# Kernel optimization log

Measured on AMD Instinct MI355X. Metric: run time of the kernel, lower is better.

## Reference

```python
import jax, jax.numpy as jnp
import numpy as np

T, D, H, E, K = 8192, 512, 1024, 16, 2  # tokens, d_model, d_hidden, num_expert, top_k


def setup_inputs() -> dict:
    key = jax.random.key(0)
    ks = jax.random.split(key, 4)
    return {
        "x": jax.random.normal(ks[0], (T, D), jnp.float32),
        "Wg": jax.random.normal(ks[1], (D, E), jnp.float32) * (D ** -0.5),
        "bg": jnp.zeros((E,), jnp.float32),
        "W1": jax.random.normal(ks[2], (E, D, H), jnp.float32) * (D ** -0.5),
        "b1": jnp.zeros((E, H), jnp.float32),
        "W2": jax.random.normal(ks[3], (E, H, D), jnp.float32) * (H ** -0.5),
        "b2": jnp.zeros((E, D), jnp.float32),
    }


def _moe(x, Wg, bg, W1, b1, W2, b2):
    # NaiveGate: linear -> top-k -> softmax over the k selected logits
    logits = x @ Wg + bg                              # [T, E]
    top_val, top_idx = jax.lax.top_k(logits, K)       # [T, K]
    score = jax.nn.softmax(top_val, axis=-1)          # [T, K]
    # Dispatch + per-expert MLP + combine. Mathematically identical to the
    # scatter/grouped-GEMM/gather: for each expert, the per-token combine
    # weight is the gate score if the token routed there, else 0.
    out = jnp.zeros_like(x)
    for e in range(E):  # fixed small loop over structurally distinct experts
        h = jax.nn.gelu(x @ W1[e] + b1[e], approximate=False)  # [T, H]
        y = h @ W2[e] + b2[e]                                   # [T, D]
        w_e = jnp.sum(jnp.where(top_idx == e, score, 0.0), axis=-1)  # [T]
        out = out + w_e[:, None] * y
    return out


def reference(x, Wg, bg, W1, b1, W2, b2):
    return _moe(x, Wg, bg, W1, b1, W2, b2)
```

## Files before the change

### kernel.cpp

```cpp
#include <hip/hip_runtime.h>
#include <hip/hip_bf16.h>
#include <math.h>

#define TT 8192
#define DD 512
#define HH 1024
#define EE 16
#define NSLOT 18432
#define MAXTILES 144
#define BM 128
#define RETRYCAP 1024

typedef __attribute__((ext_vector_type(8))) short bf16x8;
typedef __attribute__((ext_vector_type(8))) unsigned short u16x8;
typedef __attribute__((ext_vector_type(4))) float f32x4;

__device__ __forceinline__ unsigned short f2bf(float f) {
  union { float f; unsigned u; } v; v.f = f;
  unsigned r = v.u + 0x7fffu + ((v.u >> 16) & 1u);
  return (unsigned short)(r >> 16);
}

__device__ __forceinline__ float bf2f(unsigned short u) {
  union { unsigned u; float f; } v; v.u = ((unsigned)u) << 16;
  return v.f;
}

__device__ __forceinline__ void gload16(const void* g, void* l) {
  __builtin_amdgcn_global_load_lds(
      (const __attribute__((address_space(1))) unsigned int*)g,
      (__attribute__((address_space(3))) unsigned int*)l, 16, 0, 0);
}

__device__ __forceinline__ float gelu_f(float v) {
  float s = fabsf(v) * 0.70710678118654752f;
  float t = 1.0f / (1.0f + 0.3275911f * s);
  float poly = t * (0.254829592f +
              t * (-0.284496736f +
              t * (1.421413741f +
              t * (-1.453152027f +
              t * 1.061405429f))));
  float erfa = 1.0f - poly * __expf(-s * s);
  float erfv = (v >= 0.f) ? erfa : -erfa;
  return 0.5f * v * (1.0f + erfv);
}

__global__ __launch_bounds__(256) void transpose_cv_kernel(
    const float* __restrict__ in, unsigned short* __restrict__ out, int R, int C) {
  int mat = blockIdx.z;
  int c0 = blockIdx.x * 64;
  int r0 = blockIdx.y * 64;
  const float* src = in + (size_t)mat * R * C;
  unsigned short* dst = out + (size_t)mat * R * C;
  __shared__ unsigned short t[64][68];
  int tid = threadIdx.x;
#pragma unroll
  for (int p = 0; p < 4; p++) {
    int r = tid >> 2;
    int c4 = (tid & 3) + p * 4;
    float4 v = *(const float4*)(src + (size_t)(r0 + r) * C + c0 + c4 * 4);
    t[c4 * 4 + 0][r] = f2bf(v.x);
    t[c4 * 4 + 1][r] = f2bf(v.y);
    t[c4 * 4 + 2][r] = f2bf(v.z);
    t[c4 * 4 + 3][r] = f2bf(v.w);
  }
  __syncthreads();
#pragma unroll
  for (int p = 0; p < 4; p++) {
    int oc = (tid >> 4) + p * 16;
    int ch = tid & 15;
    ushort4 v = *(ushort4*)(&t[oc][ch * 4]);
    *(ushort4*)(dst + (size_t)(c0 + oc) * R + r0 + ch * 4) = v;
  }
}

__global__ __launch_bounds__(256) void gate_mfma_kernel(
    const float* __restrict__ x, const float* __restrict__ Wg,
    const float* __restrict__ bg, unsigned short* __restrict__ xb,
    int* __restrict__ gate_e, float* __restrict__ gate_w,
    int* __restrict__ counts, int* __restrict__ nretry,
    int* __restrict__ retry) {
  __shared__ __align__(16) unsigned short As[128][40];
  __shared__ int cnt_s[EE];
  int tid = threadIdx.x;
  int lane = tid & 63;
  int wave = tid >> 6;
  int tok0 = blockIdx.x * 128;
  if (tid < EE) cnt_s[tid] = 0;
  int e = lane & 15;
  int kb = (lane >> 4) * 8;
  bf16x8 bfrag[16];
#pragma unroll
  for (int ks = 0; ks < 16; ks++) {
    int kbase = ks * 32 + kb;
#pragma unroll
    for (int j = 0; j < 8; j++)
      bfrag[ks][j] = (short)f2bf(Wg[(kbase + j) * EE + e]);
  }
  float bge = bg[e];
  f32x4 acc[2];
  {
    f32x4 z = {0.f, 0.f, 0.f, 0.f};
    acc[0] = z; acc[1] = z;
  }
  int srow = tid >> 1;
  int sc0 = (tid & 1) * 16;
  const float* xrow = x + (size_t)(tok0 + srow) * DD + sc0;
  unsigned short* xbrow = xb + (size_t)(tok0 + srow) * DD + sc0;
  for (int ks = 0; ks < 16; ks++) {
    int k0 = ks * 32;
    __syncthreads();
    float4 v0 = *(const float4*)(xrow + k0);
    float4 v1 = *(const float4*)(xrow + k0 + 4);
    float4 v2 = *(const float4*)(xrow + k0 + 8);
    float4 v3 = *(const float4*)(xrow + k0 + 12);
    u16x8 w0, w1;
    w0[0] = f2bf(v0.x); w0[1] = f2bf(v0.y); w0[2] = f2bf(v0.z); w0[3] = f2bf(v0.w);
    w0[4] = f2bf(v1.x); w0[5] = f2bf(v1.y); w0[6] = f2bf(v1.z); w0[7] = f2bf(v1.w);
    w1[0] = f2bf(v2.x); w1[1] = f2bf(v2.y); w1[2] = f2bf(v2.z); w1[3] = f2bf(v2.w);
    w1[4] = f2bf(v3.x); w1[5] = f2bf(v3.y); w1[6] = f2bf(v3.z); w1[7] = f2bf(v3.w);
    *(u16x8*)(xbrow + k0) = w0;
    *(u16x8*)(xbrow + k0 + 8) = w1;
    *(u16x8*)(&As[srow][sc0]) = w0;
    *(u16x8*)(&As[srow][sc0 + 8]) = w1;
    __syncthreads();
    bf16x8 a0 = *(const bf16x8*)(&As[wave * 32 + (lane & 15)][kb]);
    bf16x8 a1 = *(const bf16x8*)(&As[wave * 32 + 16 + (lane & 15)][kb]);
    acc[0] = __builtin_amdgcn_mfma_f32_16x16x32_bf16(a0, bfrag[ks], acc[0], 0, 0, 0);
    acc[1] = __builtin_amdgcn_mfma_f32_16x16x32_bf16(a1, bfrag[ks], acc[1], 0, 0, 0);
  }
#pragma unroll
  for (int m = 0; m < 2; m++) {
#pragma unroll
    for (int r = 0; r < 4; r++) {
      float lf = acc[m][r] + bge;
      float v1 = -1e30f, v2 = -1e30f, v3 = -1e30f;
      int i1 = 0, i2 = 0;
#pragma unroll
      for (int q = 0; q < EE; q++) {
        float v = __shfl(lf, (lane & 48) | q);
        if (v > v1) { v3 = v2; v2 = v1; i2 = i1; v1 = v; i1 = q; }
        else if (v > v2) { v3 = v2; v2 = v; i2 = q; }
        else if (v > v3) { v3 = v; }
      }
      if ((lane & 15) == 0) {
        int t2 = tok0 + wave * 32 + m * 16 + ((lane >> 4) << 2) + r;
        float p = expf(v2 - v1);
        float s = 1.0f / (1.0f + p);
        gate_e[t2 * 2] = i1;
        gate_e[t2 * 2 + 1] = i2;
        gate_w[t2 * 2] = s;
        gate_w[t2 * 2 + 1] = p * s;
        atomicAdd(&cnt_s[i1], 1);
        atomicAdd(&cnt_s[i2], 1);
        if (v2 - v3 < 0.02f) {
          int pos = atomicAdd(nretry, 1);
          if (pos < RETRYCAP) retry[pos] = t2;
        }
      }
    }
  }
  __syncthreads();
  if (tid < EE) atomicAdd(&counts[tid], cnt_s[tid]);
}

__global__ __launch_bounds__(256) void gatefix_kernel(
    const float* __restrict__ x, const float* __restrict__ Wg,
    const float* __restrict__ bg, const int* __restrict__ nretry,
    const int* __restrict__ retry, int* __restrict__ gate_e,
    float* __restrict__ gate_w, int* __restrict__ counts) {
  __shared__ float lg[16][17];
  __shared__ int toks[16];
  int tid = threadIdx.x;
  int sl = tid >> 4, e = tid & 15;
  int s = blockIdx.x * 16 + sl;
  int n = *nretry; if (n > RETRYCAP) n = RETRYCAP;
  int active = (s < n);
  int tok = 0;
  if (active) tok = retry[s];
  if (active) {
    const float* xr = x + (size_t)tok * DD;
    double a0 = 0.0, a1 = 0.0, a2 = 0.0, a3 = 0.0;
    for (int i = 0; i < DD / 4; i++) {
      a0 += (double)xr[i * 4 + 0] * (double)Wg[(i * 4 + 0) * EE + e];
      a1 += (double)xr[i * 4 + 1] * (double)Wg[(i * 4 + 1) * EE + e];
      a2 += (double)xr[i * 4 + 2] * (double)Wg[(i * 4 + 2) * EE + e];
      a3 += (double)xr[i * 4 + 3] * (double)Wg[(i * 4 + 3) * EE + e];
    }
    double acc = (a0 + a1) + (a2 + a3);
    lg[sl][e] = (float)(acc + (double)bg[e]);
    toks[sl] = tok;
  }
  __syncthreads();
  if (active && e == 0) {
    float v1 = -1e30f, v2 = -1e30f;
    int i1 = 0, i2 = 0;
#pragma unroll
    for (int q = 0; q < EE; q++) {
      float v = lg[sl][q];
      if (v > v1) { v2 = v1; i2 = i1; v1 = v; i1 = q; }
      else if (v > v2) { v2 = v; i2 = q; }
    }
    int t2 = toks[sl];
    int o1 = gate_e[t2 * 2], o2 = gate_e[t2 * 2 + 1];
    float p = expf(v2 - v1);
    float sc = 1.0f / (1.0f + p);
    gate_e[t2 * 2] = i1;
    gate_e[t2 * 2 + 1] = i2;
    gate_w[t2 * 2] = sc;
    gate_w[t2 * 2 + 1] = p * sc;
    if (o1 != i1 || o2 != i2) {
      atomicSub(&counts[o1], 1);
      atomicSub(&counts[o2], 1);
      atomicAdd(&counts[i1], 1);
      atomicAdd(&counts[i2], 1);
    }
  }
}

__global__ void scan_kernel(const int* __restrict__ counts, int* __restrict__ offs,
                            int* __restrict__ tile_expert, int* __restrict__ ntiles,
                            int* __restrict__ fill) {
  if (threadIdx.x == 0) {
    int off = 0, nt = 0;
    for (int e = 0; e < EE; e++) {
      offs[e] = off;
      fill[e] = 0;
      int tiles = (counts[e] + BM - 1) / BM;
      for (int t = 0; t < tiles; t++) tile_expert[nt++] = e;
      off += tiles * BM;
    }
    offs[EE] = off;
    ntiles[0] = nt;
  }
}

__global__ __launch_bounds__(256) void scatter_kernel(
    const int* __restrict__ gate_e, const float* __restrict__ gate_w,
    const int* __restrict__ offs, int* __restrict__ fill,
    int* __restrict__ slot_token, float* __restrict__ slot_w,
    int* __restrict__ slot_of) {
  __shared__ int lcnt[EE];
  __shared__ int lbase[EE];
  int tid = threadIdx.x;
  int t = blockIdx.x * 256 + tid;
  if (tid < EE) lcnt[tid] = 0;
  __syncthreads();
  int e0 = gate_e[t * 2], e1 = gate_e[t * 2 + 1];
  int p0 = atomicAdd(&lcnt[e0], 1);
  int p1 = atomicAdd(&lcnt[e1], 1);
  __syncthreads();
  if (tid < EE) lbase[tid] = atomicAdd(&fill[tid], lcnt[tid]);
  __syncthreads();
  int s0 = offs[e0] + lbase[e0] + p0;
  int s1 = offs[e1] + lbase[e1] + p1;
  slot_token[s0] = t;
  slot_w[s0] = gate_w[t * 2];
  slot_of[t * 2] = s0;
  slot_token[s1] = t;
  slot_w[s1] = gate_w[t * 2 + 1];
  slot_of[t * 2 + 1] = s1;
}

__global__ __launch_bounds__(256) void gemm1_kernel(
    const unsigned short* __restrict__ xb, const unsigned short* __restrict__ w1t,
    const float* __restrict__ b1, const int* __restrict__ slot_token,
    const int* __restrict__ tile_expert, const int* __restrict__ ntiles,
    unsigned short* __restrict__ hb) {
  int mt = blockIdx.y;
  if (mt >= ntiles[0]) return;
  int e = tile_expert[mt];
  int row0 = mt * BM;
  int n0 = blockIdx.x * 128;
  __shared__ unsigned short As[2][128][32];
  __shared__ unsigned short Bs[2][128][32];
  int tid = threadIdx.x;
  int lane = tid & 63;
  int wave = tid >> 6;
  int wm = wave >> 1, wn = wave & 1;
  int ra = tid >> 2, c = tid & 3;
  int tok_a = slot_token[row0 + ra]; if (tok_a < 0) tok_a = 0;
  int tok_b = slot_token[row0 + ra + 64]; if (tok_b < 0) tok_b = 0;
  const unsigned short* wbase = w1t + ((size_t)e * HH * DD);
  const unsigned short* gA0 = xb + (size_t)tok_a * DD + c * 8;
  const unsigned short* gA1 = xb + (size_t)tok_b * DD + c * 8;
  const unsigned short* gB0 = wbase + (size_t)(n0 + ra) * DD + c * 8;
  const unsigned short* gB1 = wbase + (size_t)(n0 + ra + 64) * DD + c * 8;
  f32x4 acc[4][4];
#pragma unroll
  for (int m = 0; m < 4; m++)
#pragma unroll
    for (int n = 0; n < 4; n++) {
      f32x4 z = {0.f, 0.f, 0.f, 0.f};
      acc[m][n] = z;
    }
  gload16(gA0, &As[0][ra][c * 8]);
  gload16(gA1, &As[0][ra + 64][c * 8]);
  gload16(gB0, &Bs[0][ra][c * 8]);
  gload16(gB1, &Bs[0][ra + 64][c * 8]);
  int cur = 0;
  for (int kk = 0; kk < DD / 32; kk++) {
    if (kk + 1 < DD / 32) {
      int k1 = (kk + 1) * 32;
      int nx = cur ^ 1;
      gload16(gA0 + k1, &As[nx][ra][c * 8]);
      gload16(gA1 + k1, &As[nx][ra + 64][c * 8]);
      gload16(gB0 + k1, &Bs[nx][ra][c * 8]);
      gload16(gB1 + k1, &Bs[nx][ra + 64][c * 8]);
      asm volatile("s_waitcnt vmcnt(4)" ::: "memory");
    } else {
      asm volatile("s_waitcnt vmcnt(0)" ::: "memory");
    }
    __builtin_amdgcn_s_barrier();
    bf16x8 a[4], b[4];
#pragma unroll
    for (int m = 0; m < 4; m++)
      a[m] = *(const bf16x8*)(&As[cur][wm * 64 + m * 16 + (lane & 15)][(lane >> 4) * 8]);
#pragma unroll
    for (int n = 0; n < 4; n++)
      b[n] = *(const bf16x8*)(&Bs[cur][wn * 64 + n * 16 + (lane & 15)][(lane >> 4) * 8]);
#pragma unroll
    for (int m = 0; m < 4; m++)
#pragma unroll
      for (int n = 0; n < 4; n++)
        acc[m][n] = __builtin_amdgcn_mfma_f32_16x16x32_bf16(a[m], b[n], acc[m][n], 0, 0, 0);
    asm volatile("" ::: "memory");
    __builtin_amdgcn_s_barrier();
    cur ^= 1;
  }
  const float* b1e = b1 + (size_t)e * HH;
#pragma unroll
  for (int m = 0; m < 4; m++) {
#pragma unroll
    for (int r = 0; r < 4; r++) {
      int slot = row0 + wm * 64 + m * 16 + ((lane >> 4) << 2) + r;
      unsigned short* hrow = hb + (size_t)slot * HH;
#pragma unroll
      for (int n = 0; n < 4; n++) {
        int hc = n0 + wn * 64 + n * 16 + (lane & 15);
        float v = acc[m][n][r] + b1e[hc];
        hrow[hc] = f2bf(gelu_f(v));
      }
    }
  }
}

template <int USE_Y>
__global__ __launch_bounds__(256) void gemm2_kernel(
    const unsigned short* __restrict__ hb, const unsigned short* __restrict__ w2t,
    const float* __restrict__ b2, const int* __restrict__ slot_token,
    const float* __restrict__ slot_w, const int* __restrict__ tile_expert,
    const int* __restrict__ ntiles, unsigned short* __restrict__ yw,
    float* __restrict__ out) {
  int mt = blockIdx.y;
  if (mt >= ntiles[0]) return;
  int e = tile_expert[mt];
  int row0 = mt * BM;
  int n0 = blockIdx.x * 128;
  __shared__ unsigned short As[2][128][32];
  __shared__ unsigned short Bs[2][128][32];
  int tid = threadIdx.x;
  int lane = tid & 63;
  int wave = tid >> 6;
  int wm = wave >> 1, wn = wave & 1;
  int ra = tid >> 2, c = tid & 3;
  const unsigned short* wbase = w2t + ((size_t)e * DD * HH);
  const unsigned short* gA0 = hb + (size_t)(row0 + ra) * HH + c * 8;
  const unsigned short* gA1 = hb + (size_t)(row0 + ra + 64) * HH + c * 8;
  const unsigned short* gB0 = wbase + (size_t)(n0 + ra) * HH + c * 8;
  const unsigned short* gB1 = wbase + (size_t)(n0 + ra + 64) * HH + c * 8;
  f32x4 acc[4][4];
#pragma unroll
  for (int m = 0; m < 4; m++)
#pragma unroll
    for (int n = 0; n < 4; n++) {
      f32x4 z = {0.f, 0.f, 0.f, 0.f};
      acc[m][n] = z;
    }
  gload16(gA0, &As[0][ra][c * 8]);
  gload16(gA1, &As[0][ra + 64][c * 8]);
  gload16(gB0, &Bs[0][ra][c * 8]);
  gload16(gB1, &Bs[0][ra + 64][c * 8]);
  int cur = 0;
  for (int kk = 0; kk < HH / 32; kk++) {
    if (kk + 1 < HH / 32) {
      int k1 = (kk + 1) * 32;
      int nx = cur ^ 1;
      gload16(gA0 + k1, &As[nx][ra][c * 8]);
      gload16(gA1 + k1, &As[nx][ra + 64][c * 8]);
      gload16(gB0 + k1, &Bs[nx][ra][c * 8]);
      gload16(gB1 + k1, &Bs[nx][ra + 64][c * 8]);
      asm volatile("s_waitcnt vmcnt(4)" ::: "memory");
    } else {
      asm volatile("s_waitcnt vmcnt(0)" ::: "memory");
    }
    __builtin_amdgcn_s_barrier();
    bf16x8 a[4], b[4];
#pragma unroll
    for (int m = 0; m < 4; m++)
      a[m] = *(const bf16x8*)(&As[cur][wm * 64 + m * 16 + (lane & 15)][(lane >> 4) * 8]);
#pragma unroll
    for (int n = 0; n < 4; n++)
      b[n] = *(const bf16x8*)(&Bs[cur][wn * 64 + n * 16 + (lane & 15)][(lane >> 4) * 8]);
#pragma unroll
    for (int m = 0; m < 4; m++)
#pragma unroll
      for (int n = 0; n < 4; n++)
        acc[m][n] = __builtin_amdgcn_mfma_f32_16x16x32_bf16(a[m], b[n], acc[m][n], 0, 0, 0);
    asm volatile("" ::: "memory");
    __builtin_amdgcn_s_barrier();
    cur ^= 1;
  }
  const float* b2e = b2 + (size_t)e * DD;
#pragma unroll
  for (int m = 0; m < 4; m++) {
#pragma unroll
    for (int r = 0; r < 4; r++) {
      int slot = row0 + wm * 64 + m * 16 + ((lane >> 4) << 2) + r;
      if (USE_Y) {
        float w = slot_w[slot];
        unsigned short* yrow = yw + (size_t)slot * DD;
#pragma unroll
        for (int n = 0; n < 4; n++) {
          int dc = n0 + wn * 64 + n * 16 + (lane & 15);
          yrow[dc] = f2bf(w * (acc[m][n][r] + b2e[dc]));
        }
      } else {
        int tok = slot_token[slot];
        if (tok >= 0) {
          float w = slot_w[slot];
          float* orow = out + (size_t)tok * DD;
#pragma unroll
          for (int n = 0; n < 4; n++) {
            int dc = n0 + wn * 64 + n * 16 + (lane & 15);
            float v = acc[m][n][r] + b2e[dc];
            atomicAdd(&orow[dc], w * v);
          }
        }
      }
    }
  }
}

__global__ __launch_bounds__(256) void combine_kernel(
    const unsigned short* __restrict__ yw, const int* __restrict__ slot_of,
    float* __restrict__ out) {
  int gid = blockIdx.x * 256 + threadIdx.x;
  int t = gid >> 6;
  int d0 = (gid & 63) * 8;
  int s1 = slot_of[t * 2], s2 = slot_of[t * 2 + 1];
  const ushort4* p1 = (const ushort4*)(yw + (size_t)s1 * DD + d0);
  const ushort4* p2 = (const ushort4*)(yw + (size_t)s2 * DD + d0);
  ushort4 a0 = p1[0], a1 = p1[1];
  ushort4 b0 = p2[0], b1 = p2[1];
  float4 o0, o1;
  o0.x = bf2f(a0.x) + bf2f(b0.x);
  o0.y = bf2f(a0.y) + bf2f(b0.y);
  o0.z = bf2f(a0.z) + bf2f(b0.z);
  o0.w = bf2f(a0.w) + bf2f(b0.w);
  o1.x = bf2f(a1.x) + bf2f(b1.x);
  o1.y = bf2f(a1.y) + bf2f(b1.y);
  o1.z = bf2f(a1.z) + bf2f(b1.z);
  o1.w = bf2f(a1.w) + bf2f(b1.w);
  float* orow = out + (size_t)t * DD + d0;
  ((float4*)orow)[0] = o0;
  ((float4*)orow)[1] = o1;
}

extern "C" void kernel_launch(void* const* d_in, const int* in_sizes, int n_in,
                              void* d_out, int out_size, void* d_ws, size_t ws_size,
                              hipStream_t stream) {
  const float* x  = (const float*)d_in[0];
  const float* Wg = (const float*)d_in[1];
  const float* bg = (const float*)d_in[2];
  const float* W1 = (const float*)d_in[3];
  const float* b1 = (const float*)d_in[4];
  const float* W2 = (const float*)d_in[5];
  const float* b2 = (const float*)d_in[6];
  float* out = (float*)d_out;

  uint8_t* w = (uint8_t*)d_ws;
  size_t o = 0;
  unsigned short* xb  = (unsigned short*)(w + o); o += (size_t)TT * DD * 2;
  unsigned short* w1t = (unsigned short*)(w + o); o += (size_t)EE * DD * HH * 2;
  unsigned short* w2t = (unsigned short*)(w + o); o += (size_t)EE * DD * HH * 2;
  unsigned short* hb  = (unsigned short*)(w + o); o += (size_t)NSLOT * HH * 2;
  int*   slot_token = (int*)(w + o);   o += (size_t)NSLOT * 4;
  float* slot_w     = (float*)(w + o); o += (size_t)NSLOT * 4;
  int*   slot_of    = (int*)(w + o);   o += (size_t)TT * 2 * 4;
  int*   gate_e     = (int*)(w + o);   o += (size_t)TT * 2 * 4;
  float* gate_w     = (float*)(w + o); o += (size_t)TT * 2 * 4;
  int*   counts     = (int*)(w + o);   o += 64;
  int*   nretry     = (int*)(w + o);   o += 64;
  int*   tile_expert= (int*)(w + o);   o += 640;
  int*   ntiles     = (int*)(w + o);   o += 64;
  int*   offs       = (int*)(w + o);   o += 128;
  int*   fill       = (int*)(w + o);   o += 64;
  int*   retry      = (int*)(w + o);   o += RETRYCAP * 4;
  unsigned short* yw = (unsigned short*)(w + o);
  size_t need_y = o + (size_t)NSLOT * DD * 2;
  int use_y = (ws_size >= need_y);

  hipMemsetAsync(counts, 0, 128, stream);
  hipMemsetAsync(slot_token, 0xFF, (size_t)NSLOT * 4, stream);
  if (!use_y) hipMemsetAsync(d_out, 0, (size_t)TT * DD * 4, stream);

  {
    dim3 g(HH / 64, DD / 64, EE);
    transpose_cv_kernel<<<g, 256, 0, stream>>>(W1, w1t, DD, HH);
  }
  {
    dim3 g(DD / 64, HH / 64, EE);
    transpose_cv_kernel<<<g, 256, 0, stream>>>(W2, w2t, HH, DD);
  }
  gate_mfma_kernel<<<TT / 128, 256, 0, stream>>>(x, Wg, bg, xb, gate_e, gate_w,
                                                 counts, nretry, retry);
  gatefix_kernel<<<RETRYCAP / 16, 256, 0, stream>>>(x, Wg, bg, nretry, retry,
                                                    gate_e, gate_w, counts);
  scan_kernel<<<1, 64, 0, stream>>>(counts, offs, tile_expert, ntiles, fill);
  scatter_kernel<<<TT / 256, 256, 0, stream>>>(gate_e, gate_w, offs, fill,
                                               slot_token, slot_w, slot_of);
  {
    dim3 g(HH / 128, MAXTILES);
    gemm1_kernel<<<g, 256, 0, stream>>>(xb, w1t, b1, slot_token, tile_expert, ntiles, hb);
  }
  {
    dim3 g(DD / 128, MAXTILES);
    if (use_y)
      gemm2_kernel<1><<<g, 256, 0, stream>>>(hb, w2t, b2, slot_token, slot_w,
                                             tile_expert, ntiles, yw, out);
    else
      gemm2_kernel<0><<<g, 256, 0, stream>>>(hb, w2t, b2, slot_token, slot_w,
                                             tile_expert, ntiles, yw, out);
  }
  if (use_y) {
    combine_kernel<<<TT * (DD / 8) / 256, 256, 0, stream>>>(yw, slot_of, out);
  }
}
```

Before: 181.7 us.

## Triple-buffer GEMM k-loop, fuse transposes, and drop scan kernel via inline tile decode

Both grouped GEMMs move from double to triple buffering of LDS tiles, issuing loads two k-steps ahead with adjusted waitcnt so more memory latency is hidden. The two weight transpose launches are merged into one grid, and the single-thread scan kernel is removed: scatter computes expert offsets in shared memory, and the GEMMs decode their tile's expert and row offset from counts directly. This cuts kernel launches and one serial kernel. In exchange it raises LDS use per block, which may lower occupancy, and adds a small 16-iteration decode loop per block. The counts memset grows to also clear fill.

```diff
diff --git a/kernel.cpp b/kernel.cpp
--- a/kernel.cpp
+++ b/kernel.cpp
@@ -45,15 +45,38 @@
   return 0.5f * v * (1.0f + erfv);
 }
 
+__device__ __forceinline__ int tile_decode(const int* __restrict__ counts,
+                                           int mt, int* e_out, int* row0_out) {
+  int off = 0, rem = mt;
+#pragma unroll
+  for (int q = 0; q < EE; q++) {
+    int tl = (counts[q] + BM - 1) / BM;
+    if (rem < tl) { *e_out = q; *row0_out = off + rem * BM; return 1; }
+    rem -= tl;
+    off += tl * BM;
+  }
+  return 0;
+}
+
 __global__ __launch_bounds__(256) void transpose_cv_kernel(
-    const float* __restrict__ in, unsigned short* __restrict__ out, int R, int C) {
-  int mat = blockIdx.z;
-  int c0 = blockIdx.x * 64;
-  int r0 = blockIdx.y * 64;
-  const float* src = in + (size_t)mat * R * C;
-  unsigned short* dst = out + (size_t)mat * R * C;
+    const float* __restrict__ W1, const float* __restrict__ W2,
+    unsigned short* __restrict__ w1t, unsigned short* __restrict__ w2t) {
   __shared__ unsigned short t[64][68];
+  int bid = blockIdx.x;
   int tid = threadIdx.x;
+  const float* src;
+  unsigned short* dst;
+  int R, C, c0, r0;
+  if (bid < 2048) {
+    int cx = bid & 15, ry = (bid >> 4) & 7, mat = bid >> 7;
+    src = W1 + (size_t)mat * DD * HH; dst = w1t + (size_t)mat * DD * HH;
+    R = DD; C = HH; c0 = cx * 64; r0 = ry * 64;
+  } else {
+    int b = bid - 2048;
+    int cx = b & 7, ry = (b >> 3) & 15, mat = b >> 7;
+    src = W2 + (size_t)mat * DD * HH; dst = w2t + (size_t)mat * DD * HH;
+    R = HH; C = DD; c0 = cx * 64; r0 = ry * 64;
+  }
 #pragma unroll
   for (int p = 0; p < 4; p++) {
     int r = tid >> 2;
@@ -218,33 +241,24 @@
   }
 }
 
-__global__ void scan_kernel(const int* __restrict__ counts, int* __restrict__ offs,
-                            int* __restrict__ tile_expert, int* __restrict__ ntiles,
-                            int* __restrict__ fill) {
-  if (threadIdx.x == 0) {
-    int off = 0, nt = 0;
-    for (int e = 0; e < EE; e++) {
-      offs[e] = off;
-      fill[e] = 0;
-      int tiles = (counts[e] + BM - 1) / BM;
-      for (int t = 0; t < tiles; t++) tile_expert[nt++] = e;
-      off += tiles * BM;
-    }
-    offs[EE] = off;
-    ntiles[0] = nt;
-  }
-}
-
 __global__ __launch_bounds__(256) void scatter_kernel(
     const int* __restrict__ gate_e, const float* __restrict__ gate_w,
-    const int* __restrict__ offs, int* __restrict__ fill,
+    const int* __restrict__ counts, int* __restrict__ fill,
     int* __restrict__ slot_token, float* __restrict__ slot_w,
     int* __restrict__ slot_of) {
   __shared__ int lcnt[EE];
   __shared__ int lbase[EE];
+  __shared__ int offs_s[EE];
   int tid = threadIdx.x;
   int t = blockIdx.x * 256 + tid;
   if (tid < EE) lcnt[tid] = 0;
+  if (tid == 0) {
+    int off = 0;
+    for (int q = 0; q < EE; q++) {
+      offs_s[q] = off;
+      off += ((counts[q] + BM - 1) / BM) * BM;
+    }
+  }
   __syncthreads();
   int e0 = gate_e[t * 2], e1 = gate_e[t * 2 + 1];
   int p0 = atomicAdd(&lcnt[e0], 1);
@@ -252,8 +266,8 @@
   __syncthreads();
   if (tid < EE) lbase[tid] = atomicAdd(&fill[tid], lcnt[tid]);
   __syncthreads();
-  int s0 = offs[e0] + lbase[e0] + p0;
-  int s1 = offs[e1] + lbase[e1] + p1;
+  int s0 = offs_s[e0] + lbase[e0] + p0;
+  int s1 = offs_s[e1] + lbase[e1] + p1;
   slot_token[s0] = t;
   slot_w[s0] = gate_w[t * 2];
   slot_of[t * 2] = s0;
@@ -265,15 +279,12 @@
 __global__ __launch_bounds__(256) void gemm1_kernel(
     const unsigned short* __restrict__ xb, const unsigned short* __restrict__ w1t,
     const float* __restrict__ b1, const int* __restrict__ slot_token,
-    const int* __restrict__ tile_expert, const int* __restrict__ ntiles,
-    unsigned short* __restrict__ hb) {
-  int mt = blockIdx.y;
-  if (mt >= ntiles[0]) return;
-  int e = tile_expert[mt];
-  int row0 = mt * BM;
+    const int* __restrict__ counts, unsigned short* __restrict__ hb) {
+  int e, row0;
+  if (!tile_decode(counts, blockIdx.y, &e, &row0)) return;
   int n0 = blockIdx.x * 128;
-  __shared__ unsigned short As[2][128][32];
-  __shared__ unsigned short Bs[2][128][32];
+  __shared__ unsigned short As[3][128][32];
+  __shared__ unsigned short Bs[3][128][32];
   int tid = threadIdx.x;
   int lane = tid & 63;
   int wave = tid >> 6;
@@ -294,19 +305,26 @@
       f32x4 z = {0.f, 0.f, 0.f, 0.f};
       acc[m][n] = z;
     }
-  gload16(gA0, &As[0][ra][c * 8]);
-  gload16(gA1, &As[0][ra + 64][c * 8]);
-  gload16(gB0, &Bs[0][ra][c * 8]);
-  gload16(gB1, &Bs[0][ra + 64][c * 8]);
-  int cur = 0;
-  for (int kk = 0; kk < DD / 32; kk++) {
-    if (kk + 1 < DD / 32) {
-      int k1 = (kk + 1) * 32;
-      int nx = cur ^ 1;
-      gload16(gA0 + k1, &As[nx][ra][c * 8]);
-      gload16(gA1 + k1, &As[nx][ra + 64][c * 8]);
-      gload16(gB0 + k1, &Bs[nx][ra][c * 8]);
-      gload16(gB1 + k1, &Bs[nx][ra + 64][c * 8]);
+  const int NK = DD / 32;
+#pragma unroll
+  for (int p = 0; p < 2; p++) {
+    int kj = p * 32;
+    gload16(gA0 + kj, &As[p][ra][c * 8]);
+    gload16(gA1 + kj, &As[p][ra + 64][c * 8]);
+    gload16(gB0 + kj, &Bs[p][ra][c * 8]);
+    gload16(gB1 + kj, &Bs[p][ra + 64][c * 8]);
+  }
+  for (int kk = 0; kk < NK; kk++) {
+    int cur = kk % 3;
+    if (kk + 2 < NK) {
+      int k2 = (kk + 2) * 32;
+      int nx = (kk + 2) % 3;
+      gload16(gA0 + k2, &As[nx][ra][c * 8]);
+      gload16(gA1 + k2, &As[nx][ra + 64][c * 8]);
+      gload16(gB0 + k2, &Bs[nx][ra][c * 8]);
+      gload16(gB1 + k2, &Bs[nx][ra + 64][c * 8]);
+      asm volatile("s_waitcnt vmcnt(8)" ::: "memory");
+    } else if (kk + 1 < NK) {
       asm volatile("s_waitcnt vmcnt(4)" ::: "memory");
     } else {
       asm volatile("s_waitcnt vmcnt(0)" ::: "memory");
@@ -326,7 +344,6 @@
         acc[m][n] = __builtin_amdgcn_mfma_f32_16x16x32_bf16(a[m], b[n], acc[m][n], 0, 0, 0);
     asm volatile("" ::: "memory");
     __builtin_amdgcn_s_barrier();
-    cur ^= 1;
   }
   const float* b1e = b1 + (size_t)e * HH;
 #pragma unroll
@@ -349,16 +366,13 @@
 __global__ __launch_bounds__(256) void gemm2_kernel(
     const unsigned short* __restrict__ hb, const unsigned short* __restrict__ w2t,
     const float* __restrict__ b2, const int* __restrict__ slot_token,
-    const float* __restrict__ slot_w, const int* __restrict__ tile_expert,
-    const int* __restrict__ ntiles, unsigned short* __restrict__ yw,
-    float* __restrict__ out) {
-  int mt = blockIdx.y;
-  if (mt >= ntiles[0]) return;
-  int e = tile_expert[mt];
-  int row0 = mt * BM;
+    const float* __restrict__ slot_w, const int* __restrict__ counts,
+    unsigned short* __restrict__ yw, float* __restrict__ out) {
+  int e, row0;
+  if (!tile_decode(counts, blockIdx.y, &e, &row0)) return;
   int n0 = blockIdx.x * 128;
-  __shared__ unsigned short As[2][128][32];
-  __shared__ unsigned short Bs[2][128][32];
+  __shared__ unsigned short As[3][128][32];
+  __shared__ unsigned short Bs[3][128][32];
   int tid = threadIdx.x;
   int lane = tid & 63;
   int wave = tid >> 6;
@@ -377,19 +391,26 @@
       f32x4 z = {0.f, 0.f, 0.f, 0.f};
       acc[m][n] = z;
     }
-  gload16(gA0, &As[0][ra][c * 8]);
-  gload16(gA1, &As[0][ra + 64][c * 8]);
-  gload16(gB0, &Bs[0][ra][c * 8]);
-  gload16(gB1, &Bs[0][ra + 64][c * 8]);
-  int cur = 0;
-  for (int kk = 0; kk < HH / 32; kk++) {
-    if (kk + 1 < HH / 32) {
-      int k1 = (kk + 1) * 32;
-      int nx = cur ^ 1;
-      gload16(gA0 + k1, &As[nx][ra][c * 8]);
-      gload16(gA1 + k1, &As[nx][ra + 64][c * 8]);
-      gload16(gB0 + k1, &Bs[nx][ra][c * 8]);
-      gload16(gB1 + k1, &Bs[nx][ra + 64][c * 8]);
+  const int NK = HH / 32;
+#pragma unroll
+  for (int p = 0; p < 2; p++) {
+    int kj = p * 32;
+    gload16(gA0 + kj, &As[p][ra][c * 8]);
+    gload16(gA1 + kj, &As[p][ra + 64][c * 8]);
+    gload16(gB0 + kj, &Bs[p][ra][c * 8]);
+    gload16(gB1 + kj, &Bs[p][ra + 64][c * 8]);
+  }
+  for (int kk = 0; kk < NK; kk++) {
+    int cur = kk % 3;
+    if (kk + 2 < NK) {
+      int k2 = (kk + 2) * 32;
+      int nx = (kk + 2) % 3;
+      gload16(gA0 + k2, &As[nx][ra][c * 8]);
+      gload16(gA1 + k2, &As[nx][ra + 64][c * 8]);
+      gload16(gB0 + k2, &Bs[nx][ra][c * 8]);
+      gload16(gB1 + k2, &Bs[nx][ra + 64][c * 8]);
+      asm volatile("s_waitcnt vmcnt(8)" ::: "memory");
+    } else if (kk + 1 < NK) {
       asm volatile("s_waitcnt vmcnt(4)" ::: "memory");
     } else {
       asm volatile("s_waitcnt vmcnt(0)" ::: "memory");
@@ -409,7 +430,6 @@
         acc[m][n] = __builtin_amdgcn_mfma_f32_16x16x32_bf16(a[m], b[n], acc[m][n], 0, 0, 0);
     asm volatile("" ::: "memory");
     __builtin_amdgcn_s_barrier();
-    cur ^= 1;
   }
   const float* b2e = b2 + (size_t)e * DD;
 #pragma unroll
@@ -492,46 +512,35 @@
   float* gate_w     = (float*)(w + o); o += (size_t)TT * 2 * 4;
   int*   counts     = (int*)(w + o);   o += 64;
   int*   nretry     = (int*)(w + o);   o += 64;
-  int*   tile_expert= (int*)(w + o);   o += 640;
-  int*   ntiles     = (int*)(w + o);   o += 64;
-  int*   offs       = (int*)(w + o);   o += 128;
   int*   fill       = (int*)(w + o);   o += 64;
   int*   retry      = (int*)(w + o);   o += RETRYCAP * 4;
   unsigned short* yw = (unsigned short*)(w + o);
   size_t need_y = o + (size_t)NSLOT * DD * 2;
   int use_y = (ws_size >= need_y);
 
-  hipMemsetAsync(counts, 0, 128, stream);
+  hipMemsetAsync(counts, 0, 192, stream);
   hipMemsetAsync(slot_token, 0xFF, (size_t)NSLOT * 4, stream);
   if (!use_y) hipMemsetAsync(d_out, 0, (size_t)TT * DD * 4, stream);
 
-  {
-    dim3 g(HH / 64, DD / 64, EE);
-    transpose_cv_kernel<<<g, 256, 0, stream>>>(W1, w1t, DD, HH);
-  }
-  {
-    dim3 g(DD / 64, HH / 64, EE);
-    transpose_cv_kernel<<<g, 256, 0, stream>>>(W2, w2t, HH, DD);
-  }
+  transpose_cv_kernel<<<4096, 256, 0, stream>>>(W1, W2, w1t, w2t);
   gate_mfma_kernel<<<TT / 128, 256, 0, stream>>>(x, Wg, bg, xb, gate_e, gate_w,
                                                  counts, nretry, retry);
   gatefix_kernel<<<RETRYCAP / 16, 256, 0, stream>>>(x, Wg, bg, nretry, retry,
                                                     gate_e, gate_w, counts);
-  scan_kernel<<<1, 64, 0, stream>>>(counts, offs, tile_expert, ntiles, fill);
-  scatter_kernel<<<TT / 256, 256, 0, stream>>>(gate_e, gate_w, offs, fill,
+  scatter_kernel<<<TT / 256, 256, 0, stream>>>(gate_e, gate_w, counts, fill,
                                                slot_token, slot_w, slot_of);
   {
     dim3 g(HH / 128, MAXTILES);
-    gemm1_kernel<<<g, 256, 0, stream>>>(xb, w1t, b1, slot_token, tile_expert, ntiles, hb);
+    gemm1_kernel<<<g, 256, 0, stream>>>(xb, w1t, b1, slot_token, counts, hb);
   }
   {
     dim3 g(DD / 128, MAXTILES);
     if (use_y)
       gemm2_kernel<1><<<g, 256, 0, stream>>>(hb, w2t, b2, slot_token, slot_w,
-                                             tile_expert, ntiles, yw, out);
+                                             counts, yw, out);
     else
       gemm2_kernel<0><<<g, 256, 0, stream>>>(hb, w2t, b2, slot_token, slot_w,
-                                             tile_expert, ntiles, yw, out);
+                                             counts, yw, out);
   }
   if (use_y) {
     combine_kernel<<<TT * (DD / 8) / 256, 256, 0, stream>>>(yw, slot_of, out);
```

Result: faster. 177.4 us (-2.4%).
